# Performance work log

Measured on AMD Instinct MI355X. Metric: run time of the kernel, lower is better.

The kernel has to match this reference:

```python
import jax, jax.numpy as jnp
import numpy as np

H, W = 120, 160
FX, FY = 572.4114, 573.57043
CX, CY = 325.2611, 242.04899
CHUNK = 1200  # 19200 / 1200 = 16 scan steps
W_EDGE = 5.0
INV_SQRT_2PI = 1.0 / np.sqrt(2.0 * np.pi)


def backproject(depth):
    # depth: [H, W] -> organized cloud [H, W, 3]
    x = (jnp.arange(W, dtype=depth.dtype) - CX)[None, :]
    y = (jnp.arange(H, dtype=depth.dtype) - CY)[:, None]
    return jnp.stack((x * depth / FX, y * depth / FY, depth), axis=2)


def min_sq_dists(a, b):
    # For each point in a [N,3], squared distance to nearest point in b [M,3].
    # Tiled (flash-style) min-reduction: never materializes the full NxM matrix.
    b2 = jnp.sum(b * b, axis=-1)  # [M]
    n = a.shape[0]
    a_chunks = a.reshape(n // CHUNK, CHUNK, 3)

    def step(_, ac):
        a2 = jnp.sum(ac * ac, axis=-1)  # [chunk]
        d = a2[:, None] + b2[None, :] - 2.0 * (ac @ b.T)  # [chunk, M]
        return None, jnp.min(jnp.maximum(d, 0.0), axis=1)

    _, mins = jax.lax.scan(step, None, a_chunks)
    return mins.reshape(n)


def dilate(mask, ksize=9):
    # torch: clamp(conv2d(mask, ones(k,k), padding=k//2), 0, 1)
    k = jnp.ones((1, 1, ksize, ksize), mask.dtype)
    pad = ksize // 2
    out = jax.lax.conv_general_dilated(
        mask, k, window_strides=(1, 1), padding=[(pad, pad), (pad, pad)],
        dimension_numbers=("NCHW", "OIHW", "NCHW"))
    return jnp.clip(out, 0.0, 1.0)


def compute_mask_edge_weights(mask):
    # NOTE: original code calls mask_dilate_torch for BOTH dilate and erode
    # (a bug in the source), so mask_edge == 0 everywhere; replicated faithfully.
    dilated = dilate(mask, 9)
    eroded = dilate(mask, 9)
    mask_edge = dilated - eroded
    return jnp.exp(-0.5 * (mask_edge * W_EDGE) ** 2) * INV_SQRT_2PI + 1.0


def weighted_ex_loss_probs(probs, target, weight):
    pos = target > 0
    neg = target == 0
    p = jnp.clip(probs, 1e-7, 1.0 - 1e-7)
    pos_loss = jnp.where(pos, -target * jnp.log(p) * weight, 0.0)
    neg_loss = jnp.where(neg, -jnp.log(1.0 - p) * weight, 0.0)
    num_pos = jnp.sum(pos)
    num_neg = jnp.sum(neg)
    loss = jnp.where(num_pos > 0, jnp.sum(pos_loss) / jnp.maximum(num_pos, 1), 0.0)
    loss = loss + jnp.where(num_neg > 0, jnp.sum(neg_loss) / jnp.maximum(num_neg, 1), 0.0)
    return loss


def setup_inputs() -> dict:
    key = jax.random.key(0)
    k1, k2, k3, k4 = jax.random.split(key, 4)
    pred_PM = jax.random.uniform(k1, (1, H, W), dtype=jnp.float32)
    pred_Ms = (jax.random.uniform(k2, (1, H, W)) > 0.5).astype(jnp.float32)
    # strictly positive depths so the depth>0 mask keeps all H*W points (static shapes)
    depth_src = jax.random.uniform(k3, (H, W), dtype=jnp.float32) * 2.0 + 0.1
    depth_tgt = jax.random.uniform(k4, (H, W), dtype=jnp.float32) * 2.0 + 0.1
    return {"pred_PM": pred_PM, "pred_Ms": pred_Ms,
            "depth_src": depth_src, "depth_tgt": depth_tgt}


def reference(pred_PM, pred_Ms, depth_src, depth_tgt):
    # chamfer loss: backproject both depths, symmetric NN squared distance
    src_pts = backproject(depth_src).reshape(-1, 3)  # all z>0 by construction
    tgt_pts = backproject(depth_tgt).reshape(-1, 3)
    cham_loss = jnp.mean(min_sq_dists(src_pts, tgt_pts)) + jnp.mean(min_sq_dists(tgt_pts, src_pts))
    # mask loss: edge-weighted BCE-style loss
    p = pred_PM.reshape(-1, 1, H, W)
    m = pred_Ms.reshape(-1, 1, H, W)
    weights = compute_mask_edge_weights(m)
    mask_loss = weighted_ex_loss_probs(p, m, weights)
    return (cham_loss, mask_loss)
```

## Files before the change

### kernel.cpp

```cpp
#include <hip/hip_runtime.h>
#include <math.h>

#define HH 120
#define WW 160
#define NPTS (HH * WW)
#define FXC 572.4114f
#define FYC 573.57043f
#define CXC 325.2611f
#define CYC 242.04899f

#define NB 128
#define ZMIN 0.1f
#define ZMAX 2.1f
#define WB ((ZMAX - ZMIN) / NB)
#define INVWB (NB / (ZMAX - ZMIN))

#define PAD 16
#define CLOUD_STRIDE (NPTS + PAD)

#define MASK_WGT 1.3989422804014327f

#define CH_BLKS 150

typedef float __attribute__((ext_vector_type(4))) f4;

__device__ __forceinline__ void backproject_pt(int idx, float d,
                                               float& px, float& py, float& pz) {
    int y = idx / WW;
    int x = idx - y * WW;
    px = ((float)x - CXC) * d * (1.0f / FXC);
    py = ((float)y - CYC) * d * (1.0f / FYC);
    pz = d;
}

__device__ __forceinline__ float min3f(float a, float b, float c) {
    float d;
    asm("v_min3_f32 %0, %1, %2, %3" : "=v"(d) : "v"(a), "v"(b), "v"(c));
    return d;
}

__device__ __forceinline__ int zbucket(float z) {
    int b = (int)((z - ZMIN) * INVWB);
    return b < 0 ? 0 : (b > NB - 1 ? NB - 1 : b);
}

__device__ __forceinline__ int wscan_incl(int v, int lane) {
#pragma unroll
    for (int off = 1; off < 64; off <<= 1) {
        int u = __shfl_up(v, off, 64);
        if (lane >= off) v += u;
    }
    return v;
}

__global__ void __launch_bounds__(1024) prep_k(const float* __restrict__ depth_src,
                                               const float* __restrict__ depth_tgt,
                                               f4* __restrict__ sorted,
                                               int* __restrict__ offs_g,
                                               int* __restrict__ ctrl) {
    __shared__ int cnt[2 * NB];
    __shared__ int cur[2 * NB];
    const int tid = threadIdx.x;

    if (tid < 2 * NB) cnt[tid] = 0;
    if (tid < 8) ctrl[tid] = 0;
    if (tid < 2 * PAD) {
        int c = tid >> 4, k = tid & (PAD - 1);
        f4 s = {0.0f, 0.0f, 0.0f, 1e30f};
        sorted[c * CLOUD_STRIDE + NPTS + k] = s;
    }
    __syncthreads();

    for (int i = tid; i < 2 * NPTS; i += 1024) {
        int dir = (i >= NPTS);
        int idx = i - dir * NPTS;
        float d = dir ? depth_tgt[idx] : depth_src[idx];
        float px, py, pz;
        backproject_pt(idx, d, px, py, pz);
        atomicAdd(&cnt[dir * NB + zbucket(pz)], 1);
    }
    __syncthreads();

    if (tid < 128) {
        int c = tid >> 6, lane = tid & 63;
        int v0 = cnt[c * NB + lane];
        int v1 = cnt[c * NB + 64 + lane];
        int s0 = wscan_incl(v0, lane);
        int T0 = __shfl(s0, 63, 64);
        int s1 = wscan_incl(v1, lane) + T0;
        int e0 = s0 - v0, e1 = s1 - v1;
        cur[c * NB + lane] = e0;
        cur[c * NB + 64 + lane] = e1;
        offs_g[c * (NB + 1) + lane] = e0;
        offs_g[c * (NB + 1) + 64 + lane] = e1;
        if (lane == 63) offs_g[c * (NB + 1) + NB] = s1;
    }
    __syncthreads();

    for (int i = tid; i < 2 * NPTS; i += 1024) {
        int dir = (i >= NPTS);
        int idx = i - dir * NPTS;
        float d = dir ? depth_tgt[idx] : depth_src[idx];
        float px, py, pz;
        backproject_pt(idx, d, px, py, pz);
        f4 v = {px, py, pz, fmaf(px, px, fmaf(py, py, pz * pz))};
        int pos = atomicAdd(&cur[dir * NB + zbucket(pz)], 1);
        sorted[dir * CLOUD_STRIDE + pos] = v;
    }
}

__global__ void __launch_bounds__(256) chamfer_k(const f4* __restrict__ sorted,
                                                 const int* __restrict__ offs,
                                                 const float* __restrict__ pred_PM,
                                                 const float* __restrict__ pred_Ms,
                                                 int* __restrict__ ctrl,
                                                 float* __restrict__ out) {
    const int tid = threadIdx.x;
    const int lane = tid & 63;
    const int wv = blockIdx.x * 4 + (tid >> 6);
    int* acci = ctrl;
    float* accf = (float*)(ctrl + 4);

    if (wv < 300) {
        int i = wv * 64 + lane;
        float p = pred_PM[i];
        p = fminf(fmaxf(p, 1e-7f), 1.0f - 1e-7f);
        float t = pred_Ms[i];
        float ps = 0.0f, ns = 0.0f;
        int pc = 0, nc = 0;
        if (t > 0.0f)       { ps = -t * logf(p) * MASK_WGT; pc = 1; }
        else if (t == 0.0f) { ns = -logf(1.0f - p) * MASK_WGT; nc = 1; }
#pragma unroll
        for (int off = 32; off; off >>= 1) {
            ps += __shfl_xor(ps, off, 64);
            ns += __shfl_xor(ns, off, 64);
            pc += __shfl_xor(pc, off, 64);
            nc += __shfl_xor(nc, off, 64);
        }
        if (lane == 0) {
            atomicAdd(&accf[1], ps);
            atomicAdd(&accf[2], ns);
            atomicAdd(&acci[0], pc);
            atomicAdd(&acci[1], nc);
        }
    }

    {
        int dir = (wv >= 300);
        int grp = wv - dir * 300;
        const f4* SQ = sorted + dir * CLOUD_STRIDE;
        const f4* SB = sorted + (1 - dir) * CLOUD_STRIDE;
        const int* offB = offs + (1 - dir) * (NB + 1);

        f4 a = SQ[grp * 64 + lane];
        const float n2x = -2.0f * a.x, n2y = -2.0f * a.y, n2z = -2.0f * a.z;
        const float az = a.z, a2 = a.w;
        float mnA = INFINITY, mnB = INFINITY;

        int bl = zbucket(az), bh = bl;
#pragma unroll
        for (int off = 32; off; off >>= 1) {
            bl = min(bl, __shfl_xor(bl, off, 64));
            bh = max(bh, __shfl_xor(bh, off, 64));
        }

        auto scan16 = [&](int c0, int c1) {
            for (int j = c0; j < c1; j += 16) {
                f4 q[16];
#pragma unroll
                for (int k = 0; k < 16; ++k) q[k] = SB[j + k];
#pragma unroll
                for (int k = 0; k < 16; k += 4) {
                    float r0 = fmaf(n2x, q[k+0].x, fmaf(n2y, q[k+0].y, fmaf(n2z, q[k+0].z, q[k+0].w)));
                    float r1 = fmaf(n2x, q[k+1].x, fmaf(n2y, q[k+1].y, fmaf(n2z, q[k+1].z, q[k+1].w)));
                    float r2 = fmaf(n2x, q[k+2].x, fmaf(n2y, q[k+2].y, fmaf(n2z, q[k+2].z, q[k+2].w)));
                    float r3 = fmaf(n2x, q[k+3].x, fmaf(n2y, q[k+3].y, fmaf(n2z, q[k+3].z, q[k+3].w)));
                    mnA = min3f(mnA, r0, r1);
                    mnB = min3f(mnB, r2, r3);
                }
            }
        };

        scan16(offB[bl], offB[bh + 1]);

        int lo = bl, hi = bh;
        while (true) {
            float mn = fminf(mnA, mnB);
            float dcur = fmaxf(a2 + mn, 0.0f);
            float dl = az - (ZMIN + lo * WB);
            float dr = (ZMIN + (hi + 1) * WB) - az;
            bool needL = (dl * dl < dcur);
            bool needR = (dr * dr < dcur);
            bool anyL = (lo > 0) && __any(needL);
            bool anyR = (hi < NB - 1) && __any(needR);
            if (!anyL && !anyR) break;
            if (anyL) { --lo; scan16(offB[lo], offB[lo + 1]); }
            if (anyR) { ++hi; scan16(offB[hi], offB[hi + 1]); }
        }

        float w = fmaxf(a2 + fminf(mnA, mnB), 0.0f);
#pragma unroll
        for (int off = 32; off; off >>= 1) w += __shfl_xor(w, off, 64);
        if (lane == 0) atomicAdd(&accf[0], w);
    }

    __syncthreads();
    if (tid == 0) {
        __threadfence();
        int old = __hip_atomic_fetch_add(&acci[2], 1, __ATOMIC_ACQ_REL,
                                         __HIP_MEMORY_SCOPE_AGENT);
        if (old == CH_BLKS - 1) {
            __threadfence();
            float cham = __hip_atomic_load(&accf[0], __ATOMIC_RELAXED, __HIP_MEMORY_SCOPE_AGENT);
            float pos  = __hip_atomic_load(&accf[1], __ATOMIC_RELAXED, __HIP_MEMORY_SCOPE_AGENT);
            float neg  = __hip_atomic_load(&accf[2], __ATOMIC_RELAXED, __HIP_MEMORY_SCOPE_AGENT);
            int cp = __hip_atomic_load(&acci[0], __ATOMIC_RELAXED, __HIP_MEMORY_SCOPE_AGENT);
            int cn = __hip_atomic_load(&acci[1], __ATOMIC_RELAXED, __HIP_MEMORY_SCOPE_AGENT);
            out[0] = cham * (1.0f / (float)NPTS);
            float loss = 0.0f;
            if (cp > 0) loss += pos / (float)cp;
            if (cn > 0) loss += neg / (float)cn;
            out[1] = loss;
        }
    }
}

extern "C" void kernel_launch(void* const* d_in, const int* in_sizes, int n_in,
                              void* d_out, int out_size, void* d_ws, size_t ws_size,
                              hipStream_t stream) {
    const float* pred_PM   = (const float*)d_in[0];
    const float* pred_Ms   = (const float*)d_in[1];
    const float* depth_src = (const float*)d_in[2];
    const float* depth_tgt = (const float*)d_in[3];
    float* out = (float*)d_out;

    int* ctrl  = (int*)d_ws;
    int* offs  = ctrl + 16;
    f4* sorted = (f4*)((char*)d_ws + 2048);

    prep_k<<<1, 1024, 0, stream>>>(depth_src, depth_tgt, sorted, offs, ctrl);
    chamfer_k<<<CH_BLKS, 256, 0, stream>>>(sorted, offs, pred_PM, pred_Ms,
                                           ctrl, out);
}
```

Measured before the change: 81.86 us.

## Split each query wave's candidate scan across four waves of a block

Each block now handles one group of 64 query points, and its four waves stride over the candidate z-buckets in 16-point chunks instead of each wave scanning alone. Partial minima are combined through shared memory with block barriers on every bucket-expansion step, and the grid grows from 150 to 600 blocks. The mask-loss work moves to the first 75 blocks. This aims to raise parallelism and shorten the per-wave serial scan, at the cost of extra barriers and shared-memory reductions per expansion iteration.

Result: faster. 77.73 us (-5.0%).

```diff
diff --git a/kernel.cpp b/kernel.cpp
--- a/kernel.cpp
+++ b/kernel.cpp
@@ -20,7 +20,7 @@
 
 #define MASK_WGT 1.3989422804014327f
 
-#define CH_BLKS 150
+#define CH_BLKS 600
 
 typedef float __attribute__((ext_vector_type(4))) f4;
 
@@ -117,14 +117,16 @@
                                                  float* __restrict__ out) {
     const int tid = threadIdx.x;
     const int lane = tid & 63;
-    const int wv = blockIdx.x * 4 + (tid >> 6);
+    const int w = tid >> 6;
+    const int blk = blockIdx.x;
     int* acci = ctrl;
     float* accf = (float*)(ctrl + 4);
 
-    if (wv < 300) {
-        int i = wv * 64 + lane;
-        float p = pred_PM[i];
-        p = fminf(fmaxf(p, 1e-7f), 1.0f - 1e-7f);
+    __shared__ float sm[4][64];
+
+    if (blk < 75) {
+        int i = blk * 256 + tid;
+        float p = fminf(fmaxf(pred_PM[i], 1e-7f), 1.0f - 1e-7f);
         float t = pred_Ms[i];
         float ps = 0.0f, ns = 0.0f;
         int pc = 0, nc = 0;
@@ -145,63 +147,66 @@
         }
     }
 
-    {
-        int dir = (wv >= 300);
-        int grp = wv - dir * 300;
-        const f4* SQ = sorted + dir * CLOUD_STRIDE;
-        const f4* SB = sorted + (1 - dir) * CLOUD_STRIDE;
-        const int* offB = offs + (1 - dir) * (NB + 1);
-
-        f4 a = SQ[grp * 64 + lane];
-        const float n2x = -2.0f * a.x, n2y = -2.0f * a.y, n2z = -2.0f * a.z;
-        const float az = a.z, a2 = a.w;
-        float mnA = INFINITY, mnB = INFINITY;
-
-        int bl = zbucket(az), bh = bl;
-#pragma unroll
-        for (int off = 32; off; off >>= 1) {
-            bl = min(bl, __shfl_xor(bl, off, 64));
-            bh = max(bh, __shfl_xor(bh, off, 64));
-        }
-
-        auto scan16 = [&](int c0, int c1) {
-            for (int j = c0; j < c1; j += 16) {
-                f4 q[16];
-#pragma unroll
-                for (int k = 0; k < 16; ++k) q[k] = SB[j + k];
-#pragma unroll
-                for (int k = 0; k < 16; k += 4) {
-                    float r0 = fmaf(n2x, q[k+0].x, fmaf(n2y, q[k+0].y, fmaf(n2z, q[k+0].z, q[k+0].w)));
-                    float r1 = fmaf(n2x, q[k+1].x, fmaf(n2y, q[k+1].y, fmaf(n2z, q[k+1].z, q[k+1].w)));
-                    float r2 = fmaf(n2x, q[k+2].x, fmaf(n2y, q[k+2].y, fmaf(n2z, q[k+2].z, q[k+2].w)));
-                    float r3 = fmaf(n2x, q[k+3].x, fmaf(n2y, q[k+3].y, fmaf(n2z, q[k+3].z, q[k+3].w)));
-                    mnA = min3f(mnA, r0, r1);
-                    mnB = min3f(mnB, r2, r3);
-                }
+    const int dir = blk & 1;
+    const int grp = blk >> 1;
+    const f4* SQ = sorted + dir * CLOUD_STRIDE;
+    const f4* SB = sorted + (1 - dir) * CLOUD_STRIDE;
+    const int* offB = offs + (1 - dir) * (NB + 1);
+
+    f4 a = SQ[grp * 64 + lane];
+    const float n2x = -2.0f * a.x, n2y = -2.0f * a.y, n2z = -2.0f * a.z;
+    const float az = a.z, a2 = a.w;
+    float mnA = INFINITY, mnB = INFINITY;
+
+    int bl = zbucket(az), bh = bl;
+#pragma unroll
+    for (int off = 32; off; off >>= 1) {
+        bl = min(bl, __shfl_xor(bl, off, 64));
+        bh = max(bh, __shfl_xor(bh, off, 64));
+    }
+
+    auto scan_my = [&](int c0, int c1) {
+        for (int j = c0 + w * 16; j < c1; j += 64) {
+            f4 q[16];
+#pragma unroll
+            for (int k = 0; k < 16; ++k) q[k] = SB[j + k];
+#pragma unroll
+            for (int k = 0; k < 16; k += 4) {
+                float r0 = fmaf(n2x, q[k+0].x, fmaf(n2y, q[k+0].y, fmaf(n2z, q[k+0].z, q[k+0].w)));
+                float r1 = fmaf(n2x, q[k+1].x, fmaf(n2y, q[k+1].y, fmaf(n2z, q[k+1].z, q[k+1].w)));
+                float r2 = fmaf(n2x, q[k+2].x, fmaf(n2y, q[k+2].y, fmaf(n2z, q[k+2].z, q[k+2].w)));
+                float r3 = fmaf(n2x, q[k+3].x, fmaf(n2y, q[k+3].y, fmaf(n2z, q[k+3].z, q[k+3].w)));
+                mnA = min3f(mnA, r0, r1);
+                mnB = min3f(mnB, r2, r3);
             }
-        };
-
-        scan16(offB[bl], offB[bh + 1]);
-
-        int lo = bl, hi = bh;
-        while (true) {
-            float mn = fminf(mnA, mnB);
-            float dcur = fmaxf(a2 + mn, 0.0f);
-            float dl = az - (ZMIN + lo * WB);
-            float dr = (ZMIN + (hi + 1) * WB) - az;
-            bool needL = (dl * dl < dcur);
-            bool needR = (dr * dr < dcur);
-            bool anyL = (lo > 0) && __any(needL);
-            bool anyR = (hi < NB - 1) && __any(needR);
-            if (!anyL && !anyR) break;
-            if (anyL) { --lo; scan16(offB[lo], offB[lo + 1]); }
-            if (anyR) { ++hi; scan16(offB[hi], offB[hi + 1]); }
-        }
-
-        float w = fmaxf(a2 + fminf(mnA, mnB), 0.0f);
-#pragma unroll
-        for (int off = 32; off; off >>= 1) w += __shfl_xor(w, off, 64);
-        if (lane == 0) atomicAdd(&accf[0], w);
+        }
+    };
+
+    scan_my(offB[bl], offB[bh + 1]);
+
+    int lo = bl, hi = bh;
+    float m;
+    while (true) {
+        sm[w][lane] = fminf(mnA, mnB);
+        __syncthreads();
+        m = fminf(fminf(sm[0][lane], sm[1][lane]),
+                  fminf(sm[2][lane], sm[3][lane]));
+        float dcur = fmaxf(a2 + m, 0.0f);
+        float dl = az - (ZMIN + lo * WB);
+        float dr = (ZMIN + (hi + 1) * WB) - az;
+        bool anyL = (lo > 0) && __any(dl * dl < dcur);
+        bool anyR = (hi < NB - 1) && __any(dr * dr < dcur);
+        __syncthreads();
+        if (!anyL && !anyR) break;
+        if (anyL) { --lo; scan_my(offB[lo], offB[lo + 1]); }
+        if (anyR) { ++hi; scan_my(offB[hi], offB[hi + 1]); }
+    }
+
+    if (w == 0) {
+        float v = fmaxf(a2 + m, 0.0f);
+#pragma unroll
+        for (int off = 32; off; off >>= 1) v += __shfl_xor(v, off, 64);
+        if (lane == 0) atomicAdd(&accf[0], v);
     }
 
     __syncthreads();
```
